# Optimization experiments

Measured on AMD Instinct MI355X. Metric: run time of the kernel, lower is better.

Reference implementation:

```python
import jax, jax.numpy as jnp
import numpy as np

B, S, D = 2, 2048, 1024
H = 16
HD = D // H
SCALE = float(np.sqrt(HD))


def setup_inputs() -> dict:
    key = jax.random.key(0)
    ks = jax.random.split(key, 10)
    def lin(k):
        # xavier_uniform for [out, in] = [D, D]
        bound = float(np.sqrt(6.0 / (D + D)))
        return jax.random.uniform(k, (D, D), jnp.float32, -bound, bound)
    return {
        "hidden_states": jax.random.normal(ks[0], (B, S, D), jnp.float32),
        "attention_mask": jnp.ones((B, S), jnp.float32),
        "Wq": lin(ks[1]), "bq": jnp.zeros((D,), jnp.float32),
        "Wk": lin(ks[2]), "bk": jnp.zeros((D,), jnp.float32),
        "Wv": lin(ks[3]), "bv": jnp.zeros((D,), jnp.float32),
        "Wo": lin(ks[4]), "bo": jnp.zeros((D,), jnp.float32),
    }


def _heads(x):
    # [B,S,D] -> [B,H,S,HD]
    return x.reshape(B, S, H, HD).transpose(0, 2, 1, 3)


def secure_softmax(scores):
    c = jnp.clip(scores, -3.0, 3.0)
    sig = 0.5 + 0.25 * c - 0.01 * c ** 3
    sig = jnp.clip(sig, 0.01, 0.99)
    return sig / (jnp.sum(sig, axis=-1, keepdims=True) + 1e-8)


def reference(hidden_states, attention_mask, Wq, bq, Wk, bk, Wv, bv, Wo, bo):
    q = _heads(hidden_states @ Wq.T + bq)
    k = _heads(hidden_states @ Wk.T + bk)
    v = _heads(hidden_states @ Wv.T + bv)
    # [B,H,S,S]
    scores = jnp.einsum("bhqd,bhkd->bhqk", q, k) / SCALE
    scores = scores + (1.0 - attention_mask[:, None, None, :]) * -10000.0
    probs = secure_softmax(scores)
    ctx = jnp.einsum("bhqk,bhkd->bhqd", probs, v)
    ctx = ctx.transpose(0, 2, 1, 3).reshape(B, S, D)
    return ctx @ Wo.T + bo
```

## Files before the change

kernel.cpp:

```cpp
#include <hip/hip_runtime.h>
#include <stdint.h>

#define B_ 2
#define S_ 2048
#define D_ 1024
#define H_ 16
#define HD_ 64
#define M_ (B_*S_)

typedef __bf16 bf16;
typedef __attribute__((ext_vector_type(8))) __bf16 bf16x8;
typedef __attribute__((ext_vector_type(4))) float f32x4;
typedef __attribute__((ext_vector_type(2))) float f32x2;

__device__ __forceinline__ void gload16(const bf16* g, bf16* l) {
    __builtin_amdgcn_global_load_lds(
        (const __attribute__((address_space(1))) void*)g,
        (__attribute__((address_space(3))) void*)l, 16, 0, 0);
}

__global__ void k_cvt_all(const float* __restrict__ hs,
                          const float* __restrict__ Wq, const float* __restrict__ Wk,
                          const float* __restrict__ Wv, const float* __restrict__ Wo,
                          bf16* __restrict__ hb,
                          bf16* __restrict__ wqb, bf16* __restrict__ wkb,
                          bf16* __restrict__ wvb, bf16* __restrict__ wob) {
    int blk = blockIdx.x;
    const float* s; bf16* d; int base;
    if (blk < 2048) { s = hs; d = hb; base = blk; }
    else {
        int r = blk - 2048; int which = r >> 9; base = r & 511;
        s = (which==0)?Wq:(which==1)?Wk:(which==2)?Wv:Wo;
        d = (which==0)?wqb:(which==1)?wkb:(which==2)?wvb:wob;
    }
    int idx = base*2048 + threadIdx.x*8;
    float4 a = *(const float4*)(s + idx);
    float4 b = *(const float4*)(s + idx + 4);
    bf16 o[8] = {(bf16)a.x,(bf16)a.y,(bf16)a.z,(bf16)a.w,
                 (bf16)b.x,(bf16)b.y,(bf16)b.z,(bf16)b.w};
    *(int4*)(d + idx) = *(const int4*)o;
}

__global__ __launch_bounds__(256) void k_gemm_qkv(
    const bf16* __restrict__ X,
    const bf16* __restrict__ Wq, const bf16* __restrict__ Wk, const bf16* __restrict__ Wv,
    const float* __restrict__ bq, const float* __restrict__ bk, const float* __restrict__ bv,
    bf16* __restrict__ Qo, bf16* __restrict__ Ko, bf16* __restrict__ Vo)
{
    const int z = blockIdx.z;
    const bf16* W = (z==0) ? Wq : (z==1) ? Wk : Wv;
    const float* bias = (z==0) ? bq : (z==1) ? bk : bv;
    const int n0 = blockIdx.x * 128;
    const int m0 = blockIdx.y * 128;
    const int t = threadIdx.x;
    const int w = t >> 6, lane = t & 63, quad = lane >> 4, l15 = lane & 15;
    const int lr = lane >> 3;
    const int lc = (lane & 7) ^ lr;
    const int sx = l15 & 7;
    const int mw = (w >> 1) * 64, nw = (w & 1) * 64;

    __shared__ __align__(16) char smraw[128*136*2];
    bf16* As  = (bf16*)smraw;
    bf16* Bs  = (bf16*)(smraw + 16384);
    bf16* epi = (bf16*)smraw;

    f32x4 acc[4][4];
    #pragma unroll
    for (int i = 0; i < 4; i++)
        #pragma unroll
        for (int j = 0; j < 4; j++)
            acc[i][j] = (f32x4){0.f,0.f,0.f,0.f};

    const bf16* gA = X + (size_t)(m0 + w*8 + lr)*D_ + lc*8;
    const bf16* gB = W + (size_t)(n0 + w*8 + lr)*D_ + lc*8;

    for (int k0 = 0; k0 < D_; k0 += 64) {
        #pragma unroll
        for (int c = 0; c < 4; c++) {
            gload16(gA + (size_t)c*32*D_ + k0, &As[c*2048 + w*512]);
            gload16(gB + (size_t)c*32*D_ + k0, &Bs[c*2048 + w*512]);
        }
        __syncthreads();
        #pragma unroll
        for (int ks = 0; ks < 2; ks++) {
            bf16x8 af[4], bfr[4];
            #pragma unroll
            for (int i = 0; i < 4; i++)
                af[i] = *(const bf16x8*)&As[(mw + i*16 + l15)*64 + (((ks*4+quad)^sx)*8)];
            #pragma unroll
            for (int j = 0; j < 4; j++)
                bfr[j] = *(const bf16x8*)&Bs[(nw + j*16 + l15)*64 + (((ks*4+quad)^sx)*8)];
            #pragma unroll
            for (int i = 0; i < 4; i++)
                #pragma unroll
                for (int j = 0; j < 4; j++)
                    acc[i][j] = __builtin_amdgcn_mfma_f32_16x16x32_bf16(af[i], bfr[j], acc[i][j], 0, 0, 0);
        }
        __syncthreads();
    }

    const float scale = (z == 0) ? 0.125f : 1.0f;
    if (z == 2) {
        #pragma unroll
        for (int j = 0; j < 4; j++) {
            int n = nw + j*16 + l15;
            float bn = bias[n0 + n];
            #pragma unroll
            for (int i = 0; i < 4; i++) {
                int mloc = mw + i*16 + quad*4;
                union { bf16 h4[4]; uint2 u; } pk;
                #pragma unroll
                for (int r = 0; r < 4; r++) pk.h4[r] = (bf16)(acc[i][j][r] + bn);
                *(uint2*)&epi[n*136 + mloc] = pk.u;
            }
        }
    } else {
        #pragma unroll
        for (int j = 0; j < 4; j++) {
            int n = nw + j*16 + l15;
            float bn = bias[n0 + n];
            #pragma unroll
            for (int i = 0; i < 4; i++) {
                int mloc = mw + i*16 + quad*4;
                #pragma unroll
                for (int r = 0; r < 4; r++)
                    epi[(mloc + r)*136 + n] = (bf16)((acc[i][j][r] + bn) * scale);
            }
        }
    }
    __syncthreads();
    if (z == 2) {
        #pragma unroll
        for (int kk = 0; kk < 8; kk++) {
            int c = t + 256*kk;
            int row = c >> 4;
            int mcol = (c & 15) * 8;
            int4 val = *(const int4*)&epi[row*136 + mcol];
            int n = n0 + row; int hh = n >> 6, hd = n & 63;
            int m = m0 + mcol; int bb = m >> 11, s = m & 2047;
            *(int4*)&Vo[((size_t)((bb*H_ + hh)*HD_ + hd))*S_ + s] = val;
        }
    } else {
        bf16* Out = (z == 0) ? Qo : Ko;
        #pragma unroll
        for (int kk = 0; kk < 8; kk++) {
            int c = t + 256*kk;
            int row = c >> 4;
            int ncol = (c & 15) * 8;
            int4 val = *(const int4*)&epi[row*136 + ncol];
            int m = m0 + row; int bb = m >> 11, s = m & 2047;
            int n = n0 + ncol; int hh = n >> 6, hd = n & 63;
            *(int4*)&Out[((size_t)((bb*H_ + hh)*S_ + s))*HD_ + hd] = val;
        }
    }
}

__global__ __launch_bounds__(256) void k_gemm_out(
    const bf16* __restrict__ X, const bf16* __restrict__ W,
    const float* __restrict__ bias, float* __restrict__ Out)
{
    const int n0 = blockIdx.x * 128;
    const int m0 = blockIdx.y * 64;
    const int t = threadIdx.x;
    const int w = t >> 6, lane = t & 63, quad = lane >> 4, l15 = lane & 15;
    const int lr = lane >> 3;
    const int lc = (lane & 7) ^ lr;
    const int sx = l15 & 7;
    const int nw = w * 32;

    __shared__ __align__(16) bf16 As[64*64];
    __shared__ __align__(16) bf16 Bs[128*64];

    f32x4 acc[4][2];
    #pragma unroll
    for (int i = 0; i < 4; i++)
        #pragma unroll
        for (int j = 0; j < 2; j++)
            acc[i][j] = (f32x4){0.f,0.f,0.f,0.f};

    const bf16* gA = X + (size_t)(m0 + w*8 + lr)*D_ + lc*8;
    const bf16* gB = W + (size_t)(n0 + w*8 + lr)*D_ + lc*8;

    for (int k0 = 0; k0 < D_; k0 += 64) {
        #pragma unroll
        for (int c = 0; c < 2; c++)
            gload16(gA + (size_t)c*32*D_ + k0, &As[c*2048 + w*512]);
        #pragma unroll
        for (int c = 0; c < 4; c++)
            gload16(gB + (size_t)c*32*D_ + k0, &Bs[c*2048 + w*512]);
        __syncthreads();
        #pragma unroll
        for (int ks = 0; ks < 2; ks++) {
            bf16x8 af[4], bfr[2];
            #pragma unroll
            for (int i = 0; i < 4; i++)
                af[i] = *(const bf16x8*)&As[(i*16 + l15)*64 + (((ks*4+quad)^sx)*8)];
            #pragma unroll
            for (int j = 0; j < 2; j++)
                bfr[j] = *(const bf16x8*)&Bs[(nw + j*16 + l15)*64 + (((ks*4+quad)^sx)*8)];
            #pragma unroll
            for (int i = 0; i < 4; i++)
                #pragma unroll
                for (int j = 0; j < 2; j++)
                    acc[i][j] = __builtin_amdgcn_mfma_f32_16x16x32_bf16(af[i], bfr[j], acc[i][j], 0, 0, 0);
        }
        __syncthreads();
    }

    #pragma unroll
    for (int j = 0; j < 2; j++) {
        int n = n0 + nw + j*16 + l15;
        float bn = bias[n];
        #pragma unroll
        for (int i = 0; i < 4; i++) {
            int mbase = m0 + i*16 + quad*4;
            #pragma unroll
            for (int r = 0; r < 4; r++)
                Out[(size_t)(mbase + r)*D_ + n] = acc[i][j][r] + bn;
        }
    }
}

#define ATT_PAIR(BUFA, K0, PF)                                                  \
  {                                                                             \
    if (PF) {                                                                   \
      const int kp = (K0) + 128;                                                \
      _Pragma("unroll")                                                         \
      for (int c = 0; c < 2; c++) {                                             \
        gload16(KstK + (size_t)(kp + c*32)*HD_,      &Ks[(BUFA)^2][c*2048 + w*512]);     \
        gload16(VstV + (size_t)c*32*S_ + kp,         &Vs[(BUFA)^2][c*2048 + w*512]);     \
        gload16(KstK + (size_t)(kp + 64 + c*32)*HD_, &Ks[((BUFA)^2)+1][c*2048 + w*512]); \
        gload16(VstV + (size_t)c*32*S_ + kp + 64,    &Vs[((BUFA)^2)+1][c*2048 + w*512]); \
      }                                                                         \
    }                                                                           \
    f32x4 st[2][4][2];                                                          \
    _Pragma("unroll")                                                           \
    for (int sub = 0; sub < 2; sub++) {                                         \
      const int kb = (K0) + sub*64;                                             \
      _Pragma("unroll")                                                         \
      for (int g = 0; g < 4; g++) {                                             \
        float4 m4 = *(const float4*)&Ms[kb + quad*8 + (g>>1)*32 + (g&1)*4];     \
        f32x4 sti = (f32x4){m4.x, m4.y, m4.z, m4.w} * 10000.f - 10000.f;        \
        st[sub][g][0] = sti;                                                    \
        st[sub][g][1] = sti;                                                    \
      }                                                                         \
    }                                                                           \
    __builtin_amdgcn_s_setprio(1);                                              \
    _Pragma("unroll")                                                           \
    for (int sub = 0; sub < 2; sub++) {                                         \
      _Pragma("unroll")                                                         \
      for (int ks = 0; ks < 2; ks++) {                                          \
        _Pragma("unroll")                                                       \
        for (int g = 0; g < 4; g++) {                                           \
          const int kk = g >> 1, hf = g & 1;                                    \
          bf16x8 af = *(const bf16x8*)&Ks[(BUFA)+sub][(arow + hf*4 + kk*32)*64 + (((ks*4+quad)^sx)*8)]; \
          _Pragma("unroll")                                                     \
          for (int m2 = 0; m2 < 2; m2++)                                        \
            st[sub][g][m2] = __builtin_amdgcn_mfma_f32_16x16x32_bf16(af, qf[m2][ks], st[sub][g][m2], 0, 0, 0); \
        }                                                                       \
      }                                                                         \
    }                                                                           \
    __builtin_amdgcn_s_setprio(0);                                              \
    _Pragma("unroll")                                                           \
    for (int sub = 0; sub < 2; sub++) {                                         \
      const f32x2 vn3 = {-3.f, -3.f}, vp3 = {3.f, 3.f};                         \
      bf16x8 pa[2][2];                                                          \
      _Pragma("unroll")                                                         \
      for (int m2 = 0; m2 < 2; m2++) {                                          \
        _Pragma("unroll")                                                       \
        for (int kk = 0; kk < 2; kk++) {                                        \
          union { bf16 h8[8]; bf16x8 v; } pk;                                   \
          _Pragma("unroll")                                                     \
          for (int hf = 0; hf < 2; hf++) {                                      \
            f32x4 sv = st[sub][kk*2 + hf][m2];                                  \
            f32x2 lo = {sv[0], sv[1]};                                          \
            f32x2 hi = {sv[2], sv[3]};                                          \
            lo = __builtin_elementwise_min(__builtin_elementwise_max(lo, vn3), vp3); \
            hi = __builtin_elementwise_min(__builtin_elementwise_max(hi, vn3), vp3); \
            f32x2 tlo = lo * lo * (-0.01f) + 0.25f;                             \
            f32x2 thi = hi * hi * (-0.01f) + 0.25f;                             \
            f32x2 slo = lo * tlo + 0.5f;                                        \
            f32x2 shi = hi * thi + 0.5f;                                        \
            lacv[m2] += slo;                                                    \
            lacv[m2] += shi;                                                    \
            pk.h8[hf*4+0] = (bf16)slo.x; pk.h8[hf*4+1] = (bf16)slo.y;           \
            pk.h8[hf*4+2] = (bf16)shi.x; pk.h8[hf*4+3] = (bf16)shi.y;           \
          }                                                                     \
          pa[m2][kk] = pk.v;                                                    \
        }                                                                       \
      }                                                                         \
      _Pragma("unroll")                                                         \
      for (int kk = 0; kk < 2; kk++) {                                          \
        bf16x8 vf[4];                                                           \
        _Pragma("unroll")                                                       \
        for (int nt = 0; nt < 4; nt++)                                          \
          vf[nt] = *(const bf16x8*)&Vs[(BUFA)+sub][(nt*16 + l15)*64 + (((kk*4+quad)^sx)*8)]; \
        __builtin_amdgcn_s_setprio(1);                                          \
        _Pragma("unroll")                                                       \
        for (int m2 = 0; m2 < 2; m2++)                                          \
          _Pragma("unroll")                                                     \
          for (int nt = 0; nt < 4; nt++)                                        \
            cacc[m2][nt] = __builtin_amdgcn_mfma_f32_16x16x32_bf16(pa[m2][kk], vf[nt], cacc[m2][nt], 0, 0, 0); \
        __builtin_amdgcn_s_setprio(0);                                          \
      }                                                                         \
    }                                                                           \
    asm volatile("s_waitcnt vmcnt(0)\n\ts_barrier" ::: "memory");               \
  }

__global__ __launch_bounds__(256, 2) void k_attn(
    const bf16* __restrict__ Q, const bf16* __restrict__ K, const bf16* __restrict__ Vt,
    const float* __restrict__ mask, bf16* __restrict__ Ctx)
{
    const int bh = blockIdx.y;
    const int b = bh >> 4, h = bh & 15;
    const int q0 = blockIdx.x * 128;
    const int t = threadIdx.x;
    const int w = t >> 6, lane = t & 63, quad = lane >> 4, l15 = lane & 15;
    const int lr = lane >> 3;
    const int lcV = (lane & 7) ^ lr;
    const int lcK = (lane & 7) ^ ((lr & 3) | ((w & 1) << 2));
    const int sx = l15 & 7;
    const int arow = ((l15 & 12) << 1) | (l15 & 3);

    __shared__ __align__(16) bf16 Ks[4][64*64];
    __shared__ __align__(16) bf16 Vs[4][64*64];
    __shared__ __align__(16) float Ms[S_];

    bf16x8 qf[2][2];
    const bf16* Qbase = Q + ((size_t)bh*S_ + q0 + w*32)*HD_;
    #pragma unroll
    for (int m2 = 0; m2 < 2; m2++)
        #pragma unroll
        for (int ks = 0; ks < 2; ks++)
            qf[m2][ks] = *(const bf16x8*)&Qbase[(size_t)(m2*16 + l15)*HD_ + ks*32 + quad*8];

    f32x4 cacc[2][4];
    #pragma unroll
    for (int i = 0; i < 2; i++)
        #pragma unroll
        for (int j = 0; j < 4; j++)
            cacc[i][j] = (f32x4){0.f,0.f,0.f,0.f};
    f32x2 lacv[2];
    #pragma unroll
    for (int m2 = 0; m2 < 2; m2++) lacv[m2] = (f32x2){0.f,0.f};

    const bf16* KstK = K  + ((size_t)bh*S_  + w*8 + lr)*HD_ + lcK*8;
    const bf16* VstV = Vt + ((size_t)bh*HD_ + w*8 + lr)*S_  + lcV*8;

    {
        const float* mg = mask + (size_t)b*S_ + t*8;
        float4 a0 = *(const float4*)mg;
        float4 a1 = *(const float4*)(mg + 4);
        *(float4*)&Ms[t*8]     = a0;
        *(float4*)&Ms[t*8 + 4] = a1;
    }
    #pragma unroll
    for (int c = 0; c < 2; c++) {
        gload16(KstK + (size_t)(c*32)*HD_,      &Ks[0][c*2048 + w*512]);
        gload16(VstV + (size_t)c*32*S_,         &Vs[0][c*2048 + w*512]);
        gload16(KstK + (size_t)(64 + c*32)*HD_, &Ks[1][c*2048 + w*512]);
        gload16(VstV + (size_t)c*32*S_ + 64,    &Vs[1][c*2048 + w*512]);
    }
    asm volatile("s_waitcnt vmcnt(0) lgkmcnt(0)\n\ts_barrier" ::: "memory");

    for (int q2 = 0; q2 < S_/256; q2++) {
        const int k0 = q2 * 256;
        ATT_PAIR(0, k0,        true);
        ATT_PAIR(2, k0 + 128,  (q2 < S_/256 - 1));
    }

    float s[2];
    #pragma unroll
    for (int m2 = 0; m2 < 2; m2++) {
        float v = lacv[m2].x + lacv[m2].y;
        v += __shfl_xor(v, 16);
        v += __shfl_xor(v, 32);
        s[m2] = v;
    }

    #pragma unroll
    for (int m2 = 0; m2 < 2; m2++) {
        #pragma unroll
        for (int r = 0; r < 4; r++) {
            float rs = __shfl(s[m2], quad*4 + r);
            float rinv = 1.0f / (rs + 1e-8f);
            size_t row = (size_t)(b*S_ + q0 + w*32 + m2*16 + quad*4 + r);
            #pragma unroll
            for (int nt = 0; nt < 4; nt++)
                Ctx[row*D_ + h*HD_ + nt*16 + l15] = (bf16)(cacc[m2][nt][r] * rinv);
        }
    }
}

extern "C" void kernel_launch(void* const* d_in, const int* in_sizes, int n_in,
                              void* d_out, int out_size, void* d_ws, size_t ws_size,
                              hipStream_t stream) {
    const float* hs   = (const float*)d_in[0];
    const float* mask = (const float*)d_in[1];
    const float* Wq   = (const float*)d_in[2];
    const float* bq   = (const float*)d_in[3];
    const float* Wk   = (const float*)d_in[4];
    const float* bk   = (const float*)d_in[5];
    const float* Wv   = (const float*)d_in[6];
    const float* bv   = (const float*)d_in[7];
    const float* Wo   = (const float*)d_in[8];
    const float* bo   = (const float*)d_in[9];
    float* out = (float*)d_out;

    char* ws = (char*)d_ws;
    const size_t MB = 1024*1024;
    bf16* hb   = (bf16*)(ws);
    bf16* wqb  = (bf16*)(ws + 8*MB);
    bf16* wkb  = (bf16*)(ws + 10*MB);
    bf16* wvb  = (bf16*)(ws + 12*MB);
    bf16* wob  = (bf16*)(ws + 14*MB);
    bf16* qb   = (bf16*)(ws + 16*MB);
    bf16* kb   = (bf16*)(ws + 24*MB);
    bf16* vtb  = (bf16*)(ws + 32*MB);
    bf16* ctxb = (bf16*)(ws + 40*MB);

    k_cvt_all<<<2048 + 4*512, 256, 0, stream>>>(hs, Wq, Wk, Wv, Wo, hb, wqb, wkb, wvb, wob);

    k_gemm_qkv<<<dim3(D_/128, M_/128, 3), 256, 0, stream>>>(
        hb, wqb, wkb, wvb, bq, bk, bv, qb, kb, vtb);

    k_attn<<<dim3(S_/128, B_*H_), 256, 0, stream>>>(qb, kb, vtb, mask, ctxb);

    k_gemm_out<<<dim3(D_/128, M_/64), 256, 0, stream>>>(ctxb, wob, bo, out);
}
```

Baseline: 195.5 us.

## Fuse Q/K/V projections per head into one block sharing the X tile

Measured after the change: 183.7 us (median of 3 runs). 1.06x faster.

```diff
diff --git a/kernel.cpp b/kernel.cpp
--- a/kernel.cpp
+++ b/kernel.cpp
@@ -47,110 +47,122 @@
     const float* __restrict__ bq, const float* __restrict__ bk, const float* __restrict__ bv,
     bf16* __restrict__ Qo, bf16* __restrict__ Ko, bf16* __restrict__ Vo)
 {
-    const int z = blockIdx.z;
-    const bf16* W = (z==0) ? Wq : (z==1) ? Wk : Wv;
-    const float* bias = (z==0) ? bq : (z==1) ? bk : bv;
-    const int n0 = blockIdx.x * 128;
+    const int hh = blockIdx.x;
+    const int n0 = hh * 64;
     const int m0 = blockIdx.y * 128;
     const int t = threadIdx.x;
     const int w = t >> 6, lane = t & 63, quad = lane >> 4, l15 = lane & 15;
     const int lr = lane >> 3;
     const int lc = (lane & 7) ^ lr;
     const int sx = l15 & 7;
-    const int mw = (w >> 1) * 64, nw = (w & 1) * 64;
-
-    __shared__ __align__(16) char smraw[128*136*2];
+    const int mw = (w >> 1) * 64, nw = (w & 1) * 32;
+
+    __shared__ __align__(16) char smraw[40960];
     bf16* As  = (bf16*)smraw;
-    bf16* Bs  = (bf16*)(smraw + 16384);
+    bf16* Bsf = (bf16*)(smraw + 16384);
     bf16* epi = (bf16*)smraw;
 
-    f32x4 acc[4][4];
-    #pragma unroll
-    for (int i = 0; i < 4; i++)
-        #pragma unroll
-        for (int j = 0; j < 4; j++)
-            acc[i][j] = (f32x4){0.f,0.f,0.f,0.f};
+    f32x4 acc[3][4][2];
+    #pragma unroll
+    for (int z = 0; z < 3; z++)
+        #pragma unroll
+        for (int i = 0; i < 4; i++)
+            #pragma unroll
+            for (int j = 0; j < 2; j++)
+                acc[z][i][j] = (f32x4){0.f,0.f,0.f,0.f};
 
     const bf16* gA = X + (size_t)(m0 + w*8 + lr)*D_ + lc*8;
-    const bf16* gB = W + (size_t)(n0 + w*8 + lr)*D_ + lc*8;
+    const bf16* Wz[3] = {Wq, Wk, Wv};
+    const bf16* gB[6];
+    #pragma unroll
+    for (int cc = 0; cc < 6; cc++) {
+        const int z = cc >> 1;
+        const int rowz = (cc & 1)*32 + w*8 + lr;
+        gB[cc] = Wz[z] + (size_t)(n0 + rowz)*D_ + lc*8;
+    }
 
     for (int k0 = 0; k0 < D_; k0 += 64) {
         #pragma unroll
-        for (int c = 0; c < 4; c++) {
+        for (int c = 0; c < 4; c++)
             gload16(gA + (size_t)c*32*D_ + k0, &As[c*2048 + w*512]);
-            gload16(gB + (size_t)c*32*D_ + k0, &Bs[c*2048 + w*512]);
-        }
+        #pragma unroll
+        for (int cc = 0; cc < 6; cc++)
+            gload16(gB[cc] + k0, &Bsf[cc*2048 + w*512]);
         __syncthreads();
         #pragma unroll
         for (int ks = 0; ks < 2; ks++) {
-            bf16x8 af[4], bfr[4];
+            bf16x8 af[4], bfr[3][2];
             #pragma unroll
             for (int i = 0; i < 4; i++)
                 af[i] = *(const bf16x8*)&As[(mw + i*16 + l15)*64 + (((ks*4+quad)^sx)*8)];
             #pragma unroll
-            for (int j = 0; j < 4; j++)
-                bfr[j] = *(const bf16x8*)&Bs[(nw + j*16 + l15)*64 + (((ks*4+quad)^sx)*8)];
-            #pragma unroll
-            for (int i = 0; i < 4; i++)
+            for (int z = 0; z < 3; z++)
                 #pragma unroll
-                for (int j = 0; j < 4; j++)
-                    acc[i][j] = __builtin_amdgcn_mfma_f32_16x16x32_bf16(af[i], bfr[j], acc[i][j], 0, 0, 0);
-        }
-        __syncthreads();
-    }
-
-    const float scale = (z == 0) ? 0.125f : 1.0f;
-    if (z == 2) {
-        #pragma unroll
-        for (int j = 0; j < 4; j++) {
+                for (int j = 0; j < 2; j++)
+                    bfr[z][j] = *(const bf16x8*)&Bsf[z*4096 + (nw + j*16 + l15)*64 + (((ks*4+quad)^sx)*8)];
+            #pragma unroll
+            for (int z = 0; z < 3; z++)
+                #pragma unroll
+                for (int i = 0; i < 4; i++)
+                    #pragma unroll
+                    for (int j = 0; j < 2; j++)
+                        acc[z][i][j] = __builtin_amdgcn_mfma_f32_16x16x32_bf16(af[i], bfr[z][j], acc[z][i][j], 0, 0, 0);
+        }
+        __syncthreads();
+    }
+
+    #pragma unroll
+    for (int z = 0; z < 2; z++) {
+        const float scale = z ? 1.0f : 0.125f;
+        const float* bias = z ? bk : bq;
+        bf16* Out = z ? Ko : Qo;
+        #pragma unroll
+        for (int j = 0; j < 2; j++) {
             int n = nw + j*16 + l15;
             float bn = bias[n0 + n];
+            #pragma unroll
+            for (int i = 0; i < 4; i++) {
+                int mloc = mw + i*16 + quad*4;
+                #pragma unroll
+                for (int r = 0; r < 4; r++)
+                    epi[(mloc + r)*72 + n] = (bf16)((acc[z][i][j][r] + bn) * scale);
+            }
+        }
+        __syncthreads();
+        #pragma unroll
+        for (int p = 0; p < 4; p++) {
+            int c = t + 256*p;
+            int row = c >> 3;
+            int ncol = (c & 7) * 8;
+            int4 val = *(const int4*)&epi[row*72 + ncol];
+            int m = m0 + row; int bb = m >> 11, s = m & 2047;
+            *(int4*)&Out[((size_t)((bb*H_ + hh)*S_ + s))*HD_ + ncol] = val;
+        }
+        __syncthreads();
+    }
+    {
+        #pragma unroll
+        for (int j = 0; j < 2; j++) {
+            int n = nw + j*16 + l15;
+            float bn = bv[n0 + n];
             #pragma unroll
             for (int i = 0; i < 4; i++) {
                 int mloc = mw + i*16 + quad*4;
                 union { bf16 h4[4]; uint2 u; } pk;
                 #pragma unroll
-                for (int r = 0; r < 4; r++) pk.h4[r] = (bf16)(acc[i][j][r] + bn);
+                for (int r = 0; r < 4; r++) pk.h4[r] = (bf16)(acc[2][i][j][r] + bn);
                 *(uint2*)&epi[n*136 + mloc] = pk.u;
             }
         }
-    } else {
-        #pragma unroll
-        for (int j = 0; j < 4; j++) {
-            int n = nw + j*16 + l15;
-            float bn = bias[n0 + n];
-            #pragma unroll
-            for (int i = 0; i < 4; i++) {
-                int mloc = mw + i*16 + quad*4;
-                #pragma unroll
-                for (int r = 0; r < 4; r++)
-                    epi[(mloc + r)*136 + n] = (bf16)((acc[i][j][r] + bn) * scale);
-            }
-        }
-    }
-    __syncthreads();
-    if (z == 2) {
-        #pragma unroll
-        for (int kk = 0; kk < 8; kk++) {
-            int c = t + 256*kk;
+        __syncthreads();
+        #pragma unroll
+        for (int p = 0; p < 4; p++) {
+            int c = t + 256*p;
             int row = c >> 4;
             int mcol = (c & 15) * 8;
             int4 val = *(const int4*)&epi[row*136 + mcol];
-            int n = n0 + row; int hh = n >> 6, hd = n & 63;
             int m = m0 + mcol; int bb = m >> 11, s = m & 2047;
-            *(int4*)&Vo[((size_t)((bb*H_ + hh)*HD_ + hd))*S_ + s] = val;
-        }
-    } else {
-        bf16* Out = (z == 0) ? Qo : Ko;
-        #pragma unroll
-        for (int kk = 0; kk < 8; kk++) {
-            int c = t + 256*kk;
-            int row = c >> 4;
-            int ncol = (c & 15) * 8;
-            int4 val = *(const int4*)&epi[row*136 + ncol];
-            int m = m0 + row; int bb = m >> 11, s = m & 2047;
-            int n = n0 + ncol; int hh = n >> 6, hd = n & 63;
-            *(int4*)&Out[((size_t)((bb*H_ + hh)*S_ + s))*HD_ + hd] = val;
+            *(int4*)&Vo[((size_t)((bb*H_ + hh)*HD_ + row))*S_ + s] = val;
         }
     }
 }
@@ -263,7 +275,6 @@
     __builtin_amdgcn_s_setprio(0);                                              \
     _Pragma("unroll")                                                           \
     for (int sub = 0; sub < 2; sub++) {                                         \
-      const f32x2 vn3 = {-3.f, -3.f}, vp3 = {3.f, 3.f};                         \
       bf16x8 pa[2][2];                                                          \
       _Pragma("unroll")                                                         \
       for (int m2 = 0; m2 < 2; m2++) {                                          \
@@ -273,10 +284,11 @@
           _Pragma("unroll")                                                     \
           for (int hf = 0; hf < 2; hf++) {                                      \
             f32x4 sv = st[sub][kk*2 + hf][m2];                                  \
-            f32x2 lo = {sv[0], sv[1]};                                          \
-            f32x2 hi = {sv[2], sv[3]};                                          \
-            lo = __builtin_elementwise_min(__builtin_elementwise_max(lo, vn3), vp3); \
-            hi = __builtin_elementwise_min(__builtin_elementwise_max(hi, vn3), vp3); \
+            f32x2 lo, hi;                                                       \
+            lo.x = __builtin_amdgcn_fmed3f(sv[0], -3.f, 3.f);                   \
+            lo.y = __builtin_amdgcn_fmed3f(sv[1], -3.f, 3.f);                   \
+            hi.x = __builtin_amdgcn_fmed3f(sv[2], -3.f, 3.f);                   \
+            hi.y = __builtin_amdgcn_fmed3f(sv[3], -3.f, 3.f);                   \
             f32x2 tlo = lo * lo * (-0.01f) + 0.25f;                             \
             f32x2 thi = hi * hi * (-0.01f) + 0.25f;                             \
             f32x2 slo = lo * tlo + 0.5f;                                        \
@@ -421,7 +433,7 @@
 
     k_cvt_all<<<2048 + 4*512, 256, 0, stream>>>(hs, Wq, Wk, Wv, Wo, hb, wqb, wkb, wvb, wob);
 
-    k_gemm_qkv<<<dim3(D_/128, M_/128, 3), 256, 0, stream>>>(
+    k_gemm_qkv<<<dim3(H_, M_/128), 256, 0, stream>>>(
         hb, wqb, wkb, wvb, bq, bk, bv, qb, kb, vtb);
 
     k_attn<<<dim3(S_/128, B_*H_), 256, 0, stream>>>(qb, kb, vtb, mask, ctxb);
```
